# Kernel optimization log

Measured on AMD Instinct MI355X. Metric: run time of the kernel, lower is better.

Reference implementation:

```python
import jax, jax.numpy as jnp
import numpy as np

N_NODES = 50000
N_GRAPHS = 512


def gcn_conv(x, W, b, row, col, norm, n_nodes):
    # PyG GCNConv: h = x @ W; out_i = sum_{j->i} norm_ij * h_j + b
    h = x @ W  # [N, H]
    msgs = h[row] * norm[:, None]  # gather source features, scale
    out = jax.ops.segment_sum(msgs, col, num_segments=n_nodes)
    return out + b


def reference(x, edge_index, batch, W0, b0, W1, b1, W2, b2, Wf, bf):
    n = x.shape[0]
    src, dst = edge_index[0], edge_index[1]
    # add self loops
    loop = jnp.arange(n)
    row = jnp.concatenate([src, loop])
    col = jnp.concatenate([dst, loop])
    # symmetric degree normalization: 1/sqrt(deg_i * deg_j)
    deg = jax.ops.segment_sum(jnp.ones_like(col, dtype=x.dtype), col, num_segments=n)
    dis = jnp.where(deg > 0, 1.0 / jnp.sqrt(deg), 0.0)
    norm = dis[row] * dis[col]

    h = x
    for W, b in ((W0, b0), (W1, b1), (W2, b2)):
        h = jax.nn.relu(gcn_conv(h, W, b, row, col, norm, n))
        # dropout is identity in eval mode

    # global mean pool over graphs
    sums = jax.ops.segment_sum(h, batch, num_segments=N_GRAPHS)
    counts = jax.ops.segment_sum(jnp.ones((n,), dtype=h.dtype), batch, num_segments=N_GRAPHS)
    pooled = sums / jnp.maximum(counts, 1.0)[:, None]  # [B, H]

    logits = pooled @ Wf + bf
    return jax.nn.log_softmax(logits, axis=1)


def setup_inputs() -> dict:
    key = jax.random.key(0)
    ks = jax.random.split(key, 12)
    d_in, d_h, d_out = 128, 128, 10
    x = jax.random.normal(ks[0], (N_NODES, d_in), dtype=jnp.float32)
    edge_index = jax.random.randint(ks[1], (2, 600000), 0, N_NODES, dtype=jnp.int64)
    batch = jnp.sort(jax.random.randint(ks[2], (N_NODES,), 0, N_GRAPHS, dtype=jnp.int64))
    s = 1.0 / np.sqrt(d_h)
    return {
        "x": x,
        "edge_index": edge_index,
        "batch": batch,
        "W0": jax.random.normal(ks[3], (d_in, d_h), dtype=jnp.float32) * s,
        "b0": jnp.zeros((d_h,), dtype=jnp.float32),
        "W1": jax.random.normal(ks[4], (d_h, d_h), dtype=jnp.float32) * s,
        "b1": jnp.zeros((d_h,), dtype=jnp.float32),
        "W2": jax.random.normal(ks[5], (d_h, d_h), dtype=jnp.float32) * s,
        "b2": jnp.zeros((d_h,), dtype=jnp.float32),
        "Wf": jax.random.normal(ks[6], (d_h, d_out), dtype=jnp.float32) * s,
        "bf": jnp.zeros((d_out,), dtype=jnp.float32),
    }
```

## Files before the change

### kernel.cpp

```cpp
#include <hip/hip_runtime.h>
#include <hip/hip_bf16.h>

#define NN 50000
#define NE 600000
#define NG 512

typedef __attribute__((ext_vector_type(8))) short bf16x8;
typedef __attribute__((ext_vector_type(4))) float f32x4;

__device__ __forceinline__ float bf_lo(unsigned u) {
    unsigned v = u << 16;
    return __builtin_bit_cast(float, v);
}
__device__ __forceinline__ float bf_hi(unsigned u) {
    unsigned v = u & 0xFFFF0000u;
    return __builtin_bit_cast(float, v);
}
__device__ __forceinline__ unsigned f2bf(float f) {
    unsigned u = __builtin_bit_cast(unsigned, f);
    return (u + 0x7FFFu + ((u >> 16) & 1u)) >> 16;
}

__global__ __launch_bounds__(256) void k_zero(float* p, int n) {
    int i = blockIdx.x * 256 + threadIdx.x;
    if (i < n) p[i] = 0.0f;
}

__global__ __launch_bounds__(256) void k_hist(const int* __restrict__ dst, int* __restrict__ deg) {
    int e = blockIdx.x * 256 + threadIdx.x;
    if (e < NE) atomicAdd(&deg[dst[e]], 1);
}

__global__ __launch_bounds__(256) void k_counts(const int* __restrict__ batch, float* __restrict__ counts) {
    int i = blockIdx.x * 256 + threadIdx.x;
    if (i < NN) atomicAdd(&counts[batch[i]], 1.0f);
}

__global__ __launch_bounds__(256) void k_alloc(const int* __restrict__ deg, int* __restrict__ gcur,
                                               int* __restrict__ rowstart, int* __restrict__ cursor,
                                               float* __restrict__ dis, uint2* __restrict__ cpk) {
    int i = blockIdx.x * 256 + threadIdx.x;
    if (i >= NN) return;
    int d = deg[i];
    int dr = (d + 3) & ~3;
    int st = atomicAdd(gcur, dr);
    rowstart[i] = st;
    cursor[i] = st;
    dis[i] = 1.0f / sqrtf((float)(d + 1));
    for (int p = st + d; p < st + dr; ++p) cpk[p] = make_uint2(0u, 0u);
}

__global__ __launch_bounds__(256) void k_fill(const int* __restrict__ src, const int* __restrict__ dst,
                                              const float* __restrict__ dis, int* __restrict__ cursor,
                                              uint2* __restrict__ cpk) {
    int e = blockIdx.x * 256 + threadIdx.x;
    if (e >= NE) return;
    int s = src[e], d = dst[e];
    int slot = atomicAdd(&cursor[d], 1);
    cpk[slot] = make_uint2((unsigned)s, __builtin_bit_cast(unsigned, dis[s] * dis[d]));
}

__global__ __launch_bounds__(256) void k_cvt_x(const float4* __restrict__ in, uint2* __restrict__ out, int n4) {
    int i = blockIdx.x * 256 + threadIdx.x;
    if (i >= n4) return;
    float4 v = in[i];
    uint2 o;
    o.x = f2bf(v.x) | (f2bf(v.y) << 16);
    o.y = f2bf(v.z) | (f2bf(v.w) << 16);
    out[i] = o;
}

__global__ __launch_bounds__(256) void k_cvt_w(const float* __restrict__ W0, const float* __restrict__ W1,
                                               const float* __restrict__ W2, unsigned short* __restrict__ Wt) {
    int idx = blockIdx.x * 256 + threadIdx.x;
    if (idx >= 3 * 16384) return;
    int m = idx >> 14;
    int r = idx & 16383;
    int k = r >> 7, c = r & 127;
    const float* W = (m == 0) ? W0 : (m == 1) ? W1 : W2;
    Wt[m * 16384 + c * 128 + k] = (unsigned short)f2bf(W[k * 128 + c]);
}

__global__ __launch_bounds__(256) void k_gemm_mfma(const unsigned short* __restrict__ A,
                                                   const unsigned short* __restrict__ Wt,
                                                   unsigned short* __restrict__ C, int M) {
    int wave = threadIdx.x >> 6;
    int lane = threadIdx.x & 63;
    int rowbase = blockIdx.x * 64 + wave * 16;
    int lr = lane & 15;
    int kg = lane >> 4;

    int arow = rowbase + lr;
    if (arow >= M) arow = M - 1;
    bf16x8 a[4];
#pragma unroll
    for (int kt = 0; kt < 4; ++kt)
        a[kt] = *(const bf16x8*)&A[arow * 128 + kt * 32 + kg * 8];

    f32x4 acc[8];
#pragma unroll
    for (int nt = 0; nt < 8; ++nt) acc[nt] = (f32x4){0.f, 0.f, 0.f, 0.f};

#pragma unroll
    for (int nt = 0; nt < 8; ++nt) {
        const unsigned short* wp = &Wt[(nt * 16 + lr) * 128 + kg * 8];
#pragma unroll
        for (int kt = 0; kt < 4; ++kt) {
            bf16x8 b = *(const bf16x8*)&wp[kt * 32];
            acc[nt] = __builtin_amdgcn_mfma_f32_16x16x32_bf16(a[kt], b, acc[nt], 0, 0, 0);
        }
    }

    int crow0 = rowbase + (lane >> 4) * 4;
#pragma unroll
    for (int nt = 0; nt < 8; ++nt) {
#pragma unroll
        for (int r = 0; r < 4; ++r) {
            int gr = crow0 + r;
            if (gr < M) C[gr * 128 + nt * 16 + lr] = (unsigned short)f2bf(acc[nt][r]);
        }
    }
}

template <int POOL>
__global__ __launch_bounds__(256) void k_gather(const uint2* __restrict__ h,
                                                const int* __restrict__ rowstart,
                                                const int* __restrict__ rowend,
                                                const uint2* __restrict__ cpk,
                                                const float* __restrict__ dis,
                                                const float* __restrict__ bias,
                                                uint2* __restrict__ outbuf,
                                                const int* __restrict__ batch,
                                                float* __restrict__ sums) {
    int t = blockIdx.x * 256 + threadIdx.x;
    int node = t >> 5;
    if (node >= NN) return;
    int f = t & 31;

    int s0 = rowstart[node];
    int e0 = rowend[node];

    float A0 = 0.f, A1 = 0.f, A2 = 0.f, A3 = 0.f;
    float B0 = 0.f, B1 = 0.f, B2 = 0.f, B3 = 0.f;
    float C0 = 0.f, C1 = 0.f, C2 = 0.f, C3 = 0.f;
    float D0 = 0.f, D1 = 0.f, D2 = 0.f, D3 = 0.f;

    for (int s = s0; s < e0; s += 4) {
        uint4 q01 = *(const uint4*)&cpk[s];
        uint4 q23 = *(const uint4*)&cpk[s + 2];
        uint2 v0 = h[(int)q01.x * 32 + f];
        uint2 v1 = h[(int)q01.z * 32 + f];
        uint2 v2 = h[(int)q23.x * 32 + f];
        uint2 v3 = h[(int)q23.z * 32 + f];
        float w0 = __builtin_bit_cast(float, q01.y);
        float w1 = __builtin_bit_cast(float, q01.w);
        float w2 = __builtin_bit_cast(float, q23.y);
        float w3 = __builtin_bit_cast(float, q23.w);
        A0 = fmaf(bf_lo(v0.x), w0, A0);
        A1 = fmaf(bf_hi(v0.x), w0, A1);
        A2 = fmaf(bf_lo(v0.y), w0, A2);
        A3 = fmaf(bf_hi(v0.y), w0, A3);
        B0 = fmaf(bf_lo(v1.x), w1, B0);
        B1 = fmaf(bf_hi(v1.x), w1, B1);
        B2 = fmaf(bf_lo(v1.y), w1, B2);
        B3 = fmaf(bf_hi(v1.y), w1, B3);
        C0 = fmaf(bf_lo(v2.x), w2, C0);
        C1 = fmaf(bf_hi(v2.x), w2, C1);
        C2 = fmaf(bf_lo(v2.y), w2, C2);
        C3 = fmaf(bf_hi(v2.y), w2, C3);
        D0 = fmaf(bf_lo(v3.x), w3, D0);
        D1 = fmaf(bf_hi(v3.x), w3, D1);
        D2 = fmaf(bf_lo(v3.y), w3, D2);
        D3 = fmaf(bf_hi(v3.y), w3, D3);
    }

    float d = dis[node];
    float w0 = d * d;
    uint2 hv = h[node * 32 + f];
    A0 = fmaf(bf_lo(hv.x), w0, A0);
    A1 = fmaf(bf_hi(hv.x), w0, A1);
    A2 = fmaf(bf_lo(hv.y), w0, A2);
    A3 = fmaf(bf_hi(hv.y), w0, A3);

    float a0 = (A0 + B0) + (C0 + D0);
    float a1 = (A1 + B1) + (C1 + D1);
    float a2 = (A2 + B2) + (C2 + D2);
    float a3 = (A3 + B3) + (C3 + D3);

    float4 b = ((const float4*)bias)[f];
    a0 = fmaxf(a0 + b.x, 0.f);
    a1 = fmaxf(a1 + b.y, 0.f);
    a2 = fmaxf(a2 + b.z, 0.f);
    a3 = fmaxf(a3 + b.w, 0.f);

    if (POOL == 0) {
        uint2 o;
        o.x = f2bf(a0) | (f2bf(a1) << 16);
        o.y = f2bf(a2) | (f2bf(a3) << 16);
        outbuf[node * 32 + f] = o;
    } else {
        int g = batch[node];
        float* o = sums + g * 128 + f * 4;
        atomicAdd(o + 0, a0);
        atomicAdd(o + 1, a1);
        atomicAdd(o + 2, a2);
        atomicAdd(o + 3, a3);
    }
}

__global__ __launch_bounds__(64) void k_head(const float* __restrict__ sums,
                                             const float* __restrict__ counts,
                                             const float* __restrict__ Wf,
                                             const float* __restrict__ bf,
                                             float* __restrict__ out) {
    int g = blockIdx.x;
    int l = threadIdx.x;
    float inv = 1.0f / fmaxf(counts[g], 1.0f);
    float p0 = sums[g * 128 + l] * inv;
    float p1 = sums[g * 128 + 64 + l] * inv;
    float logit[10];
#pragma unroll
    for (int o = 0; o < 10; ++o) {
        float part = p0 * Wf[l * 10 + o] + p1 * Wf[(l + 64) * 10 + o];
#pragma unroll
        for (int s = 32; s > 0; s >>= 1) part += __shfl_xor(part, s);
        logit[o] = part + bf[o];
    }
    if (l == 0) {
        float m = logit[0];
#pragma unroll
        for (int o = 1; o < 10; ++o) m = fmaxf(m, logit[o]);
        float sum = 0.f;
#pragma unroll
        for (int o = 0; o < 10; ++o) sum += expf(logit[o] - m);
        float lse = m + logf(sum);
#pragma unroll
        for (int o = 0; o < 10; ++o) out[g * 10 + o] = logit[o] - lse;
    }
}

extern "C" void kernel_launch(void* const* d_in, const int* in_sizes, int n_in,
                              void* d_out, int out_size, void* d_ws, size_t ws_size,
                              hipStream_t stream) {
    const float* x     = (const float*)d_in[0];
    const int*   ei    = (const int*)d_in[1];
    const int*   batch = (const int*)d_in[2];
    const float* W0 = (const float*)d_in[3];
    const float* b0 = (const float*)d_in[4];
    const float* W1 = (const float*)d_in[5];
    const float* b1 = (const float*)d_in[6];
    const float* W2 = (const float*)d_in[7];
    const float* b2 = (const float*)d_in[8];
    const float* Wf = (const float*)d_in[9];
    const float* bf = (const float*)d_in[10];
    float* out = (float*)d_out;

    float* ws = (float*)d_ws;
    float* sums    = ws;
    float* counts  = ws + 65536;
    int*   in_deg  = (int*)(ws + 66048);
    int*   gcur    = (int*)(ws + 116096);
    float* dis     = ws + 116160;
    int*   rowstart= (int*)(ws + 166208);
    int*   cursor  = (int*)(ws + 216256);
    uint2* cpk     = (uint2*)(ws + 266304);
    unsigned short* Wt = (unsigned short*)(ws + 1866432);
    unsigned short* bx = (unsigned short*)(ws + 1891008);
    unsigned short* hA = (unsigned short*)(ws + 5091008);
    unsigned short* hB = (unsigned short*)(ws + 8291008);

    const int* src = ei;
    const int* dst = ei + NE;

    k_zero<<<(116160 + 255) / 256, 256, 0, stream>>>(ws, 116160);
    k_hist<<<2344, 256, 0, stream>>>(dst, in_deg);
    k_counts<<<196, 256, 0, stream>>>(batch, counts);
    k_alloc<<<196, 256, 0, stream>>>(in_deg, gcur, rowstart, cursor, dis, cpk);
    k_fill<<<2344, 256, 0, stream>>>(src, dst, dis, cursor, cpk);
    k_cvt_x<<<6250, 256, 0, stream>>>((const float4*)x, (uint2*)bx, NN * 32);
    k_cvt_w<<<192, 256, 0, stream>>>(W0, W1, W2, Wt);

    const int GEMM_GRID = (NN + 63) / 64;

    k_gemm_mfma<<<GEMM_GRID, 256, 0, stream>>>(bx, Wt, hB, NN);
    k_gather<0><<<6250, 256, 0, stream>>>((const uint2*)hB, rowstart, cursor, cpk,
                                          dis, b0, (uint2*)hA, batch, sums);
    k_gemm_mfma<<<GEMM_GRID, 256, 0, stream>>>(hA, Wt + 16384, hB, NN);
    k_gather<0><<<6250, 256, 0, stream>>>((const uint2*)hB, rowstart, cursor, cpk,
                                          dis, b1, (uint2*)hA, batch, sums);
    k_gemm_mfma<<<GEMM_GRID, 256, 0, stream>>>(hA, Wt + 32768, hB, NN);
    k_gather<1><<<6250, 256, 0, stream>>>((const uint2*)hB, rowstart, cursor, cpk,
                                          dis, b2, nullptr, batch, sums);

    k_head<<<512, 64, 0, stream>>>(sums, counts, Wf, bf, out);
}
```

Measured before the change: 363.4 us.

## Split gather feature columns into XCD-aligned chunks for per-XCD L2 locality

```diff
diff --git a/kernel.cpp b/kernel.cpp
--- a/kernel.cpp
+++ b/kernel.cpp
@@ -123,88 +123,72 @@
 }
 
 template <int POOL>
-__global__ __launch_bounds__(256) void k_gather(const uint2* __restrict__ h,
+__global__ __launch_bounds__(256) void k_gather(const unsigned* __restrict__ h,
                                                 const int* __restrict__ rowstart,
                                                 const int* __restrict__ rowend,
                                                 const uint2* __restrict__ cpk,
                                                 const float* __restrict__ dis,
                                                 const float* __restrict__ bias,
-                                                uint2* __restrict__ outbuf,
+                                                unsigned* __restrict__ outbuf,
                                                 const int* __restrict__ batch,
                                                 float* __restrict__ sums) {
-    int t = blockIdx.x * 256 + threadIdx.x;
-    int node = t >> 5;
+    int pair = blockIdx.x >> 3;
+    int xcd = blockIdx.x & 7;
+    int chunk = xcd >> 1;
+    int half = xcd & 1;
+    int node = pair * 32 + half * 16 + (threadIdx.x >> 4);
     if (node >= NN) return;
-    int f = t & 31;
+    int sl = threadIdx.x & 15;
+    int cbase = chunk * 16 + sl;
 
     int s0 = rowstart[node];
     int e0 = rowend[node];
 
-    float A0 = 0.f, A1 = 0.f, A2 = 0.f, A3 = 0.f;
-    float B0 = 0.f, B1 = 0.f, B2 = 0.f, B3 = 0.f;
-    float C0 = 0.f, C1 = 0.f, C2 = 0.f, C3 = 0.f;
-    float D0 = 0.f, D1 = 0.f, D2 = 0.f, D3 = 0.f;
+    float A0 = 0.f, A1 = 0.f, B0 = 0.f, B1 = 0.f;
+    float C0 = 0.f, C1 = 0.f, D0 = 0.f, D1 = 0.f;
 
     for (int s = s0; s < e0; s += 4) {
         uint4 q01 = *(const uint4*)&cpk[s];
         uint4 q23 = *(const uint4*)&cpk[s + 2];
-        uint2 v0 = h[(int)q01.x * 32 + f];
-        uint2 v1 = h[(int)q01.z * 32 + f];
-        uint2 v2 = h[(int)q23.x * 32 + f];
-        uint2 v3 = h[(int)q23.z * 32 + f];
+        unsigned v0 = h[(int)q01.x * 64 + cbase];
+        unsigned v1 = h[(int)q01.z * 64 + cbase];
+        unsigned v2 = h[(int)q23.x * 64 + cbase];
+        unsigned v3 = h[(int)q23.z * 64 + cbase];
         float w0 = __builtin_bit_cast(float, q01.y);
         float w1 = __builtin_bit_cast(float, q01.w);
         float w2 = __builtin_bit_cast(float, q23.y);
         float w3 = __builtin_bit_cast(float, q23.w);
-        A0 = fmaf(bf_lo(v0.x), w0, A0);
-        A1 = fmaf(bf_hi(v0.x), w0, A1);
-        A2 = fmaf(bf_lo(v0.y), w0, A2);
-        A3 = fmaf(bf_hi(v0.y), w0, A3);
-        B0 = fmaf(bf_lo(v1.x), w1, B0);
-        B1 = fmaf(bf_hi(v1.x), w1, B1);
-        B2 = fmaf(bf_lo(v1.y), w1, B2);
-        B3 = fmaf(bf_hi(v1.y), w1, B3);
-        C0 = fmaf(bf_lo(v2.x), w2, C0);
-        C1 = fmaf(bf_hi(v2.x), w2, C1);
-        C2 = fmaf(bf_lo(v2.y), w2, C2);
-        C3 = fmaf(bf_hi(v2.y), w2, C3);
-        D0 = fmaf(bf_lo(v3.x), w3, D0);
-        D1 = fmaf(bf_hi(v3.x), w3, D1);
-        D2 = fmaf(bf_lo(v3.y), w3, D2);
-        D3 = fmaf(bf_hi(v3.y), w3, D3);
+        A0 = fmaf(bf_lo(v0), w0, A0);
+        A1 = fmaf(bf_hi(v0), w0, A1);
+        B0 = fmaf(bf_lo(v1), w1, B0);
+        B1 = fmaf(bf_hi(v1), w1, B1);
+        C0 = fmaf(bf_lo(v2), w2, C0);
+        C1 = fmaf(bf_hi(v2), w2, C1);
+        D0 = fmaf(bf_lo(v3), w3, D0);
+        D1 = fmaf(bf_hi(v3), w3, D1);
     }
 
     float d = dis[node];
-    float w0 = d * d;
-    uint2 hv = h[node * 32 + f];
-    A0 = fmaf(bf_lo(hv.x), w0, A0);
-    A1 = fmaf(bf_hi(hv.x), w0, A1);
-    A2 = fmaf(bf_lo(hv.y), w0, A2);
-    A3 = fmaf(bf_hi(hv.y), w0, A3);
+    float ws = d * d;
+    unsigned hv = h[node * 64 + cbase];
+    A0 = fmaf(bf_lo(hv), ws, A0);
+    A1 = fmaf(bf_hi(hv), ws, A1);
 
     float a0 = (A0 + B0) + (C0 + D0);
     float a1 = (A1 + B1) + (C1 + D1);
-    float a2 = (A2 + B2) + (C2 + D2);
-    float a3 = (A3 + B3) + (C3 + D3);
-
-    float4 b = ((const float4*)bias)[f];
+
+    float2 b = ((const float2*)bias)[cbase];
     a0 = fmaxf(a0 + b.x, 0.f);
     a1 = fmaxf(a1 + b.y, 0.f);
-    a2 = fmaxf(a2 + b.z, 0.f);
-    a3 = fmaxf(a3 + b.w, 0.f);
 
     if (POOL == 0) {
-        uint2 o;
-        o.x = f2bf(a0) | (f2bf(a1) << 16);
-        o.y = f2bf(a2) | (f2bf(a3) << 16);
-        outbuf[node * 32 + f] = o;
+        unsigned o = f2bf(a0) | (f2bf(a1) << 16);
+        outbuf[node * 64 + cbase] = o;
     } else {
         int g = batch[node];
-        float* o = sums + g * 128 + f * 4;
+        float* o = sums + g * 128 + cbase * 2;
         atomicAdd(o + 0, a0);
         atomicAdd(o + 1, a1);
-        atomicAdd(o + 2, a2);
-        atomicAdd(o + 3, a3);
     }
 }
 
@@ -281,16 +265,17 @@
     k_cvt_w<<<192, 256, 0, stream>>>(W0, W1, W2, Wt);
 
     const int GEMM_GRID = (NN + 63) / 64;
+    const int GATHER_GRID = ((NN + 31) / 32) * 8;
 
     k_gemm_mfma<<<GEMM_GRID, 256, 0, stream>>>(bx, Wt, hB, NN);
-    k_gather<0><<<6250, 256, 0, stream>>>((const uint2*)hB, rowstart, cursor, cpk,
-                                          dis, b0, (uint2*)hA, batch, sums);
+    k_gather<0><<<GATHER_GRID, 256, 0, stream>>>((const unsigned*)hB, rowstart, cursor, cpk,
+                                                 dis, b0, (unsigned*)hA, batch, sums);
     k_gemm_mfma<<<GEMM_GRID, 256, 0, stream>>>(hA, Wt + 16384, hB, NN);
-    k_gather<0><<<6250, 256, 0, stream>>>((const uint2*)hB, rowstart, cursor, cpk,
-                                          dis, b1, (uint2*)hA, batch, sums);
+    k_gather<0><<<GATHER_GRID, 256, 0, stream>>>((const unsigned*)hB, rowstart, cursor, cpk,
+                                                 dis, b1, (unsigned*)hA, batch, sums);
     k_gemm_mfma<<<GEMM_GRID, 256, 0, stream>>>(hA, Wt + 32768, hB, NN);
-    k_gather<1><<<6250, 256, 0, stream>>>((const uint2*)hB, rowstart, cursor, cpk,
-                                          dis, b2, nullptr, batch, sums);
+    k_gather<1><<<GATHER_GRID, 256, 0, stream>>>((const unsigned*)hB, rowstart, cursor, cpk,
+                                                 dis, b2, nullptr, batch, sums);
 
     k_head<<<512, 64, 0, stream>>>(sums, counts, Wf, bf, out);
 }
```

Result: slower. 395.3 us (+8.8%).
